# Kernel optimization log

Measured on AMD Instinct MI355X. Metric: run time of the kernel, lower is better.

Reference implementation:

```python
import jax, jax.numpy as jnp
import numpy as np

N_NODES = 100000


def _gcn_conv(x, edge_index, W, b, n_nodes):
    # PyG GCNConv with add_self_loops=True, default gcn_norm:
    #   out = D^{-1/2} (A + I) D^{-1/2} (x @ W) + b
    xw = x @ W  # [N, out_dim]
    src = jnp.concatenate([edge_index[0], jnp.arange(n_nodes)])
    dst = jnp.concatenate([edge_index[1], jnp.arange(n_nodes)])
    ones = jnp.ones(src.shape[0], dtype=x.dtype)
    deg = jax.ops.segment_sum(ones, dst, num_segments=n_nodes)  # includes self loops
    dinv = jnp.where(deg > 0, jax.lax.rsqrt(deg), 0.0)
    norm = dinv[src] * dinv[dst]  # [E + N]
    msgs = xw[src] * norm[:, None]  # gather + scale per edge
    out = jax.ops.segment_sum(msgs, dst, num_segments=n_nodes)
    return out + b


def setup_inputs() -> dict:
    key = jax.random.key(0)
    k1, k2, k3, k4 = jax.random.split(key, 4)
    N, E = N_NODES, 1600000
    in_dim, hid_dim, out_dim = 128, 128, 64
    x = jax.random.normal(k1, (N, in_dim), dtype=jnp.float32)
    edge_index = jax.random.randint(k2, (2, E), 0, N, dtype=jnp.int64)
    W1 = jax.random.normal(k3, (in_dim, hid_dim), dtype=jnp.float32) * (1.0 / np.sqrt(in_dim))
    b1 = jnp.zeros((hid_dim,), dtype=jnp.float32)
    W2 = jax.random.normal(k4, (hid_dim, out_dim), dtype=jnp.float32) * (1.0 / np.sqrt(hid_dim))
    b2 = jnp.zeros((out_dim,), dtype=jnp.float32)
    return {"x": x, "edge_index": edge_index, "W1": W1, "b1": b1, "W2": W2, "b2": b2}


def reference(x, edge_index, W1, b1, W2, b2):
    h = _gcn_conv(x, edge_index, W1, b1, N_NODES)
    out = _gcn_conv(h, edge_index, W2, b2, N_NODES)
    return out
```

## Files before the change

kernel.cpp:

```cpp
#include <hip/hip_runtime.h>

#define NNODES 100000
#define NBUCK ((NNODES + 127) >> 7)
#define CAPB 3072
#define BINCAP 16
#define GFILL 256

__device__ __forceinline__ float bf2f(unsigned short u) {
    unsigned int v = ((unsigned int)u) << 16;
    return __builtin_bit_cast(float, v);
}
__device__ __forceinline__ unsigned short f2bf(float f) {
    unsigned int u = __builtin_bit_cast(unsigned int, f);
    u += 0x7FFF + ((u >> 16) & 1);
    return (unsigned short)(u >> 16);
}


__global__ __launch_bounds__(512) void fill_wc(const int* __restrict__ ei, int E,
                                               int* __restrict__ gcur,
                                               int* __restrict__ seg) {
    __shared__ int lcnt[NBUCK];
    __shared__ int lbin[NBUCK * BINCAP];

    const int t = threadIdx.x;
    for (int i = t; i < NBUCK; i += 512) lcnt[i] = 0;
    __syncthreads();

    const int per = (E + GFILL - 1) / GFILL;
    const int e0 = blockIdx.x * per;
    const int e1 = min(e0 + per, E);

    for (int base = e0; base < e1; base += 512) {
        int e = base + t;
        if (e < e1) {
            int src = ei[e];
            int d = ei[E + e];
            int b = (unsigned)d >> 7;
            int p = (src << 7) | (d & 127);
            int pos = atomicAdd(&lcnt[b], 1);
            if (pos < BINCAP) {
                lbin[b * BINCAP + pos] = p;
            } else {
                int gp = atomicAdd(&gcur[b << 4], 1);
                if (gp < CAPB) seg[b * CAPB + gp] = p;
            }
        }
        __syncthreads();
        for (int bb = t; bb < NBUCK; bb += 512) {
            if (lcnt[bb] >= BINCAP) {
                int gp = atomicAdd(&gcur[bb << 4], BINCAP);
                if (gp + BINCAP <= CAPB) {
                    int* dp = seg + bb * CAPB + gp;
                    const int* sp = lbin + bb * BINCAP;
#pragma unroll
                    for (int j = 0; j < BINCAP; ++j) dp[j] = sp[j];
                }
                lcnt[bb] = 0;
            }
        }
        __syncthreads();
    }
    for (int bb = t; bb < NBUCK; bb += 512) {
        int c = min(lcnt[bb], BINCAP);
        if (c > 0) {
            int gp = atomicAdd(&gcur[bb << 4], c);
            int* dp = seg + bb * CAPB;
            const int* sp = lbin + bb * BINCAP;
            for (int j = 0; j < c && gp + j < CAPB; ++j) dp[gp + j] = sp[j];
        }
    }
}


__global__ __launch_bounds__(256) void stats_kernel(const int* __restrict__ gcur,
                                                    const int* __restrict__ seg,
                                                    float* __restrict__ dinv, int N) {
    __shared__ int cnt[128];
    const int t = threadIdx.x, b = blockIdx.x;
    if (t < 128) cnt[t] = 0;
    __syncthreads();
    int c = min(gcur[b << 4], CAPB);
    const int* sp = seg + b * CAPB;
    for (int i = t; i < c; i += 256) atomicAdd(&cnt[sp[i] & 127], 1);
    __syncthreads();
    int node = (b << 7) + t;
    if (t < 128 && node < N) dinv[node] = rsqrtf((float)cnt[t] + 1.0f);
}


__global__ __launch_bounds__(256) void w12_kernel(const float* __restrict__ W1,
                                                  const float* __restrict__ b1,
                                                  const float* __restrict__ W2,
                                                  float* __restrict__ W12,
                                                  float* __restrict__ bW2) {
    int j = threadIdx.x % 64;
    int r = threadIdx.x / 64;
    if (blockIdx.x < 32) {
        int i = blockIdx.x * 4 + r;
        float acc = 0.f;
        for (int k = 0; k < 128; ++k) acc += W1[i * 128 + k] * W2[k * 64 + j];
        W12[i * 64 + j] = acc;
    } else if (r == 0) {
        float acc = 0.f;
        for (int k = 0; k < 128; ++k) acc += b1[k] * W2[k * 64 + j];
        bW2[j] = acc;
    }
}


__global__ __launch_bounds__(256) void gemm_scale_bf(const float* __restrict__ X,
                                                     const float* __restrict__ W,
                                                     const float* __restrict__ dinv,
                                                     unsigned short* __restrict__ Ybf, int N) {
    constexpr int K = 128;
    constexpr int KP = K + 4;
    constexpr int OD = 64;
    constexpr int JG = OD / 4;
    constexpr int TR = 256 / JG;
    constexpr int ROWS = TR * 4;

    __shared__ float sW[K * OD];
    __shared__ float sX[ROWS * KP];

    const int tid = threadIdx.x;

    for (int i = tid; i < K * OD / 4; i += 256)
        ((float4*)sW)[i] = ((const float4*)W)[i];

    const int jg = tid % JG;
    const int tr = tid / JG;
    const int r0 = tr * 4;
    const int base = blockIdx.x * ROWS;

    const int k4 = (tid & 31) * 4;
    for (int rl = tid >> 5; rl < ROWS; rl += 8) {
        int row = base + rl;
        float4 v = make_float4(0.f, 0.f, 0.f, 0.f);
        if (row < N) v = *(const float4*)(X + (size_t)row * K + k4);
        *(float4*)(sX + rl * KP + k4) = v;
    }
    __syncthreads();

    float acc[4][4] = {{0.f}};
#pragma unroll 8
    for (int k = 0; k < K; ++k) {
        float4 w = *(const float4*)(sW + k * OD + jg * 4);
        float x0 = sX[(r0 + 0) * KP + k];
        float x1 = sX[(r0 + 1) * KP + k];
        float x2 = sX[(r0 + 2) * KP + k];
        float x3 = sX[(r0 + 3) * KP + k];
        acc[0][0] += x0 * w.x; acc[0][1] += x0 * w.y; acc[0][2] += x0 * w.z; acc[0][3] += x0 * w.w;
        acc[1][0] += x1 * w.x; acc[1][1] += x1 * w.y; acc[1][2] += x1 * w.z; acc[1][3] += x1 * w.w;
        acc[2][0] += x2 * w.x; acc[2][1] += x2 * w.y; acc[2][2] += x2 * w.z; acc[2][3] += x2 * w.w;
        acc[3][0] += x3 * w.x; acc[3][1] += x3 * w.y; acc[3][2] += x3 * w.z; acc[3][3] += x3 * w.w;
    }

#pragma unroll
    for (int i = 0; i < 4; ++i) {
        int row = base + r0 + i;
        if (row < N) {
            float sc = dinv[row];
            ushort4 o;
            o.x = f2bf(acc[i][0] * sc);
            o.y = f2bf(acc[i][1] * sc);
            o.z = f2bf(acc[i][2] * sc);
            o.w = f2bf(acc[i][3] * sc);
            *(ushort4*)(Ybf + (size_t)row * OD + jg * 4) = o;
        }
    }
}


template <bool FINAL>
__global__ __launch_bounds__(256) void agg_sort(const int* __restrict__ gcur,
                                                const int* __restrict__ seg,
                                                const unsigned short* __restrict__ Y,
                                                const float* __restrict__ dinv,
                                                const float* __restrict__ bW2,
                                                const float* __restrict__ b2,
                                                unsigned short* __restrict__ out_bf,
                                                float* __restrict__ out_f, int N) {
    __shared__ int el[CAPB];
    __shared__ int csr[CAPB];
    __shared__ int cnt[128], sh[128], rs[128], cur[128];

    const int t = threadIdx.x, b = blockIdx.x;
    const int total = min(gcur[b << 4], CAPB);

    if (t < 128) cnt[t] = 0;
    __syncthreads();
    {
        const int* sp = seg + b * CAPB;
        for (int i = t; i < total; i += 256) el[i] = sp[i];
    }
    __syncthreads();

    for (int i = t; i < total; i += 256) atomicAdd(&cnt[el[i] & 127], 1);
    __syncthreads();
    int v = (t < 128) ? cnt[t] : 0;
    if (t < 128) sh[t] = v;
    __syncthreads();
    for (int offp = 1; offp < 128; offp <<= 1) {
        int u = (t < 128 && t >= offp) ? sh[t - offp] : 0;
        __syncthreads();
        if (t < 128) sh[t] += u;
        __syncthreads();
    }
    if (t < 128) {
        int excl = sh[t] - v;
        rs[t] = excl;
        cur[t] = excl;
    }
    __syncthreads();
    for (int i = t; i < total; i += 256) {
        int p = el[i];
        int pos = atomicAdd(&cur[p & 127], 1);
        csr[pos] = (int)((unsigned)p >> 7);
    }
    __syncthreads();

    const int g = t >> 4, lane = t & 15, c4 = lane * 4;
    const int base = b << 7;

    for (int nl = g; nl < 128; nl += 16) {
        int node = base + nl;
        if (node >= N) continue;

        ushort4 sv = *(const ushort4*)(Y + (size_t)node * 64 + c4);
        float ax = bf2f(sv.x), ay = bf2f(sv.y), az = bf2f(sv.z), aw = bf2f(sv.w);
        float ds = 0.f;

        const int s0 = rs[nl];
        const int e0 = s0 + cnt[nl];
        int i = s0;
        for (; i + 4 <= e0; i += 4) {
            int a0 = csr[i + 0];
            int a1 = csr[i + 1];
            int a2 = csr[i + 2];
            int a3 = csr[i + 3];
            ushort4 v0 = *(const ushort4*)(Y + (size_t)a0 * 64 + c4);
            ushort4 v1 = *(const ushort4*)(Y + (size_t)a1 * 64 + c4);
            ushort4 v2 = *(const ushort4*)(Y + (size_t)a2 * 64 + c4);
            ushort4 v3 = *(const ushort4*)(Y + (size_t)a3 * 64 + c4);
            ax += bf2f(v0.x) + bf2f(v1.x) + bf2f(v2.x) + bf2f(v3.x);
            ay += bf2f(v0.y) + bf2f(v1.y) + bf2f(v2.y) + bf2f(v3.y);
            az += bf2f(v0.z) + bf2f(v1.z) + bf2f(v2.z) + bf2f(v3.z);
            aw += bf2f(v0.w) + bf2f(v1.w) + bf2f(v2.w) + bf2f(v3.w);
            if (FINAL && lane == 0)
                ds += dinv[a0] + dinv[a1] + dinv[a2] + dinv[a3];
        }
        for (; i < e0; ++i) {
            int a = csr[i];
            ushort4 vv = *(const ushort4*)(Y + (size_t)a * 64 + c4);
            ax += bf2f(vv.x); ay += bf2f(vv.y); az += bf2f(vv.z); aw += bf2f(vv.w);
            if (FINAL && lane == 0) ds += dinv[a];
        }

        float di = rsqrtf((float)cnt[nl] + 1.0f);
        if (FINAL) {
            float dsg = __shfl(ds, (g << 4), 64);
            float si = di * (di + dsg);
            float4 bb = *(const float4*)(bW2 + c4);
            float4 bv = *(const float4*)(b2 + c4);
            float4 o;
            o.x = di * ax + si * bb.x + bv.x;
            o.y = di * ay + si * bb.y + bv.y;
            o.z = di * az + si * bb.z + bv.z;
            o.w = di * aw + si * bb.w + bv.w;
            *(float4*)(out_f + (size_t)node * 64 + c4) = o;
        } else {
            float d2 = di * di;
            ushort4 o;
            o.x = f2bf(d2 * ax);
            o.y = f2bf(d2 * ay);
            o.z = f2bf(d2 * az);
            o.w = f2bf(d2 * aw);
            *(ushort4*)(out_bf + (size_t)node * 64 + c4) = o;
        }
    }
}


extern "C" void kernel_launch(void* const* d_in, const int* in_sizes, int n_in,
                              void* d_out, int out_size, void* d_ws, size_t ws_size,
                              hipStream_t stream) {
    const float* x  = (const float*)d_in[0];
    const int*   ei = (const int*)d_in[1];
    const float* W1 = (const float*)d_in[2];
    const float* b1 = (const float*)d_in[3];
    const float* W2 = (const float*)d_in[4];
    const float* b2 = (const float*)d_in[5];
    float* out = (float*)d_out;

    const int N = NNODES;
    const int E = in_sizes[1] / 2;

    float* ws   = (float*)d_ws;
    float* dinv = ws;
    float* W12  = dinv + N;
    float* bW2  = W12 + 8192;
    unsigned short* ybf = (unsigned short*)(bW2 + 64);
    unsigned short* zbf = ybf + (size_t)N * 64;
    int*  seg  = (int*)(zbf + (size_t)N * 64);
    int*  gcur = seg + (size_t)NBUCK * CAPB;

    hipMemsetAsync(gcur, 0, (size_t)NBUCK * 16 * sizeof(int), stream);

    fill_wc<<<GFILL, 512, 0, stream>>>(ei, E, gcur, seg);
    w12_kernel<<<33, 256, 0, stream>>>(W1, b1, W2, W12, bW2);
    stats_kernel<<<NBUCK, 256, 0, stream>>>(gcur, seg, dinv, N);

    gemm_scale_bf<<<(N + 63) / 64, 256, 0, stream>>>(x, W12, dinv, ybf, N);
    agg_sort<false><<<NBUCK, 256, 0, stream>>>(gcur, seg, ybf, dinv, nullptr, nullptr, zbf, nullptr, N);
    agg_sort<true><<<NBUCK, 256, 0, stream>>>(gcur, seg, zbf, dinv, bW2, b2, nullptr, out, N);
}
```

Measured before the change: 261.6 us.

## Sort buckets once into CSR, pipeline gathers, stream X directly in GEMM

```diff
diff --git a/kernel.cpp b/kernel.cpp
--- a/kernel.cpp
+++ b/kernel.cpp
@@ -73,19 +73,60 @@
 }
 
 
-__global__ __launch_bounds__(256) void stats_kernel(const int* __restrict__ gcur,
-                                                    const int* __restrict__ seg,
-                                                    float* __restrict__ dinv, int N) {
-    __shared__ int cnt[128];
+__global__ __launch_bounds__(512) void sortseg(const int* __restrict__ gcur,
+                                               int* __restrict__ seg,
+                                               float* __restrict__ dinv,
+                                               int* __restrict__ rsb,
+                                               int* __restrict__ cntb, int N) {
+    __shared__ int el[CAPB];
+    __shared__ int csr[CAPB];
+    __shared__ int cnt[128], sh[128], rs[128], cur[128];
+
     const int t = threadIdx.x, b = blockIdx.x;
+    const int total = min(gcur[b << 4], CAPB);
+
     if (t < 128) cnt[t] = 0;
     __syncthreads();
-    int c = min(gcur[b << 4], CAPB);
-    const int* sp = seg + b * CAPB;
-    for (int i = t; i < c; i += 256) atomicAdd(&cnt[sp[i] & 127], 1);
-    __syncthreads();
-    int node = (b << 7) + t;
-    if (t < 128 && node < N) dinv[node] = rsqrtf((float)cnt[t] + 1.0f);
+    {
+        const int* sp = seg + b * CAPB;
+        for (int i = t; i < total; i += 512) el[i] = sp[i];
+    }
+    __syncthreads();
+
+    for (int i = t; i < total; i += 512) atomicAdd(&cnt[el[i] & 127], 1);
+    __syncthreads();
+    int v = (t < 128) ? cnt[t] : 0;
+    if (t < 128) sh[t] = v;
+    __syncthreads();
+    for (int offp = 1; offp < 128; offp <<= 1) {
+        int u = (t < 128 && t >= offp) ? sh[t - offp] : 0;
+        __syncthreads();
+        if (t < 128) sh[t] += u;
+        __syncthreads();
+    }
+    if (t < 128) {
+        int excl = sh[t] - v;
+        rs[t] = excl;
+        cur[t] = excl;
+    }
+    __syncthreads();
+    for (int i = t; i < total; i += 512) {
+        int p = el[i];
+        int pos = atomicAdd(&cur[p & 127], 1);
+        csr[pos] = (int)((unsigned)p >> 7);
+    }
+    __syncthreads();
+
+    {
+        int* dp = seg + b * CAPB;
+        for (int i = t; i < total; i += 512) dp[i] = csr[i];
+    }
+    if (t < 128) {
+        rsb[b * 128 + t] = rs[t];
+        cntb[b * 128 + t] = cnt[t];
+        int node = (b << 7) + t;
+        if (node < N) dinv[node] = rsqrtf((float)cnt[t] + 1.0f);
+    }
 }
 
 
@@ -114,116 +155,90 @@
                                                      const float* __restrict__ dinv,
                                                      unsigned short* __restrict__ Ybf, int N) {
     constexpr int K = 128;
-    constexpr int KP = K + 4;
     constexpr int OD = 64;
-    constexpr int JG = OD / 4;
-    constexpr int TR = 256 / JG;
-    constexpr int ROWS = TR * 4;
 
     __shared__ float sW[K * OD];
-    __shared__ float sX[ROWS * KP];
 
     const int tid = threadIdx.x;
-
     for (int i = tid; i < K * OD / 4; i += 256)
         ((float4*)sW)[i] = ((const float4*)W)[i];
-
-    const int jg = tid % JG;
-    const int tr = tid / JG;
-    const int r0 = tr * 4;
-    const int base = blockIdx.x * ROWS;
-
-    const int k4 = (tid & 31) * 4;
-    for (int rl = tid >> 5; rl < ROWS; rl += 8) {
-        int row = base + rl;
-        float4 v = make_float4(0.f, 0.f, 0.f, 0.f);
-        if (row < N) v = *(const float4*)(X + (size_t)row * K + k4);
-        *(float4*)(sX + rl * KP + k4) = v;
-    }
-    __syncthreads();
+    __syncthreads();
+
+    const int jg = tid & 15;
+    const int tr = tid >> 4;
+    const int r0 = blockIdx.x * 64 + tr * 4;
+
+    const float* xr[4];
+#pragma unroll
+    for (int r = 0; r < 4; ++r) xr[r] = X + (size_t)min(r0 + r, N - 1) * K;
 
     float acc[4][4] = {{0.f}};
-#pragma unroll 8
-    for (int k = 0; k < K; ++k) {
-        float4 w = *(const float4*)(sW + k * OD + jg * 4);
-        float x0 = sX[(r0 + 0) * KP + k];
-        float x1 = sX[(r0 + 1) * KP + k];
-        float x2 = sX[(r0 + 2) * KP + k];
-        float x3 = sX[(r0 + 3) * KP + k];
-        acc[0][0] += x0 * w.x; acc[0][1] += x0 * w.y; acc[0][2] += x0 * w.z; acc[0][3] += x0 * w.w;
-        acc[1][0] += x1 * w.x; acc[1][1] += x1 * w.y; acc[1][2] += x1 * w.z; acc[1][3] += x1 * w.w;
-        acc[2][0] += x2 * w.x; acc[2][1] += x2 * w.y; acc[2][2] += x2 * w.z; acc[2][3] += x2 * w.w;
-        acc[3][0] += x3 * w.x; acc[3][1] += x3 * w.y; acc[3][2] += x3 * w.z; acc[3][3] += x3 * w.w;
-    }
-
-#pragma unroll
-    for (int i = 0; i < 4; ++i) {
-        int row = base + r0 + i;
+#pragma unroll 2
+    for (int k = 0; k < K; k += 4) {
+        float4 xv[4];
+#pragma unroll
+        for (int r = 0; r < 4; ++r) xv[r] = *(const float4*)(xr[r] + k);
+#pragma unroll
+        for (int kk = 0; kk < 4; ++kk) {
+            float4 w = *(const float4*)(sW + (k + kk) * OD + (jg << 2));
+#pragma unroll
+            for (int r = 0; r < 4; ++r) {
+                float xs = (&xv[r].x)[kk];
+                acc[r][0] += xs * w.x;
+                acc[r][1] += xs * w.y;
+                acc[r][2] += xs * w.z;
+                acc[r][3] += xs * w.w;
+            }
+        }
+    }
+
+#pragma unroll
+    for (int r = 0; r < 4; ++r) {
+        int row = r0 + r;
         if (row < N) {
             float sc = dinv[row];
             ushort4 o;
-            o.x = f2bf(acc[i][0] * sc);
-            o.y = f2bf(acc[i][1] * sc);
-            o.z = f2bf(acc[i][2] * sc);
-            o.w = f2bf(acc[i][3] * sc);
-            *(ushort4*)(Ybf + (size_t)row * OD + jg * 4) = o;
+            o.x = f2bf(acc[r][0] * sc);
+            o.y = f2bf(acc[r][1] * sc);
+            o.z = f2bf(acc[r][2] * sc);
+            o.w = f2bf(acc[r][3] * sc);
+            *(ushort4*)(Ybf + (size_t)row * OD + (jg << 2)) = o;
         }
     }
 }
 
 
 template <bool FINAL>
-__global__ __launch_bounds__(256) void agg_sort(const int* __restrict__ gcur,
-                                                const int* __restrict__ seg,
-                                                const unsigned short* __restrict__ Y,
-                                                const float* __restrict__ dinv,
-                                                const float* __restrict__ bW2,
-                                                const float* __restrict__ b2,
-                                                unsigned short* __restrict__ out_bf,
-                                                float* __restrict__ out_f, int N) {
-    __shared__ int el[CAPB];
-    __shared__ int csr[CAPB];
-    __shared__ int cnt[128], sh[128], rs[128], cur[128];
+__global__ __launch_bounds__(512) void agg_csr(const int* __restrict__ seg,
+                                               const int* __restrict__ rsb,
+                                               const int* __restrict__ cntb,
+                                               const unsigned short* __restrict__ Y,
+                                               const float* __restrict__ dinv,
+                                               const float* __restrict__ bW2,
+                                               const float* __restrict__ b2,
+                                               unsigned short* __restrict__ out_bf,
+                                               float* __restrict__ out_f, int N) {
+    __shared__ int csrS[CAPB];
+    __shared__ int rsS[128], cntS[128];
 
     const int t = threadIdx.x, b = blockIdx.x;
-    const int total = min(gcur[b << 4], CAPB);
-
-    if (t < 128) cnt[t] = 0;
-    __syncthreads();
+
+    if (t < 128) {
+        rsS[t] = rsb[b * 128 + t];
+        cntS[t] = cntb[b * 128 + t];
+    }
+    __syncthreads();
+    const int total = rsS[127] + cntS[127];
     {
         const int* sp = seg + b * CAPB;
-        for (int i = t; i < total; i += 256) el[i] = sp[i];
-    }
-    __syncthreads();
-
-    for (int i = t; i < total; i += 256) atomicAdd(&cnt[el[i] & 127], 1);
-    __syncthreads();
-    int v = (t < 128) ? cnt[t] : 0;
-    if (t < 128) sh[t] = v;
-    __syncthreads();
-    for (int offp = 1; offp < 128; offp <<= 1) {
-        int u = (t < 128 && t >= offp) ? sh[t - offp] : 0;
-        __syncthreads();
-        if (t < 128) sh[t] += u;
-        __syncthreads();
-    }
-    if (t < 128) {
-        int excl = sh[t] - v;
-        rs[t] = excl;
-        cur[t] = excl;
-    }
-    __syncthreads();
-    for (int i = t; i < total; i += 256) {
-        int p = el[i];
-        int pos = atomicAdd(&cur[p & 127], 1);
-        csr[pos] = (int)((unsigned)p >> 7);
+        for (int i = t; i < total; i += 512) csrS[i] = sp[i];
     }
     __syncthreads();
 
     const int g = t >> 4, lane = t & 15, c4 = lane * 4;
     const int base = b << 7;
 
-    for (int nl = g; nl < 128; nl += 16) {
+    for (int nl = g; nl < 128; nl += 32) {
         int node = base + nl;
         if (node >= N) continue;
 
@@ -231,36 +246,65 @@
         float ax = bf2f(sv.x), ay = bf2f(sv.y), az = bf2f(sv.z), aw = bf2f(sv.w);
         float ds = 0.f;
 
-        const int s0 = rs[nl];
-        const int e0 = s0 + cnt[nl];
+        const int s0 = rsS[nl];
+        const int ne = cntS[nl];
+        const int e0 = s0 + ne;
         int i = s0;
-        for (; i + 4 <= e0; i += 4) {
-            int a0 = csr[i + 0];
-            int a1 = csr[i + 1];
-            int a2 = csr[i + 2];
-            int a3 = csr[i + 3];
-            ushort4 v0 = *(const ushort4*)(Y + (size_t)a0 * 64 + c4);
-            ushort4 v1 = *(const ushort4*)(Y + (size_t)a1 * 64 + c4);
-            ushort4 v2 = *(const ushort4*)(Y + (size_t)a2 * 64 + c4);
-            ushort4 v3 = *(const ushort4*)(Y + (size_t)a3 * 64 + c4);
-            ax += bf2f(v0.x) + bf2f(v1.x) + bf2f(v2.x) + bf2f(v3.x);
-            ay += bf2f(v0.y) + bf2f(v1.y) + bf2f(v2.y) + bf2f(v3.y);
-            az += bf2f(v0.z) + bf2f(v1.z) + bf2f(v2.z) + bf2f(v3.z);
-            aw += bf2f(v0.w) + bf2f(v1.w) + bf2f(v2.w) + bf2f(v3.w);
-            if (FINAL && lane == 0)
-                ds += dinv[a0] + dinv[a1] + dinv[a2] + dinv[a3];
+        const int nch = ne >> 3;
+
+        if (nch > 0) {
+            ushort4 buf[8];
+            float dv = 0.f;
+#pragma unroll
+            for (int j = 0; j < 8; ++j)
+                buf[j] = *(const ushort4*)(Y + (size_t)csrS[s0 + j] * 64 + c4);
+            if (FINAL && lane < 8) dv = dinv[csrS[s0 + lane]];
+
+            for (int c = 1; c < nch; ++c) {
+                const int ib = s0 + (c << 3);
+                ushort4 nb[8];
+#pragma unroll
+                for (int j = 0; j < 8; ++j)
+                    nb[j] = *(const ushort4*)(Y + (size_t)csrS[ib + j] * 64 + c4);
+                float ndv = 0.f;
+                if (FINAL && lane < 8) ndv = dinv[csrS[ib + lane]];
+#pragma unroll
+                for (int j = 0; j < 8; ++j) {
+                    ax += bf2f(buf[j].x);
+                    ay += bf2f(buf[j].y);
+                    az += bf2f(buf[j].z);
+                    aw += bf2f(buf[j].w);
+                }
+                ds += dv;
+#pragma unroll
+                for (int j = 0; j < 8; ++j) buf[j] = nb[j];
+                dv = ndv;
+            }
+#pragma unroll
+            for (int j = 0; j < 8; ++j) {
+                ax += bf2f(buf[j].x);
+                ay += bf2f(buf[j].y);
+                az += bf2f(buf[j].z);
+                aw += bf2f(buf[j].w);
+            }
+            ds += dv;
+            i = s0 + (nch << 3);
         }
         for (; i < e0; ++i) {
-            int a = csr[i];
+            int a = csrS[i];
             ushort4 vv = *(const ushort4*)(Y + (size_t)a * 64 + c4);
             ax += bf2f(vv.x); ay += bf2f(vv.y); az += bf2f(vv.z); aw += bf2f(vv.w);
             if (FINAL && lane == 0) ds += dinv[a];
         }
 
-        float di = rsqrtf((float)cnt[nl] + 1.0f);
+        float di = rsqrtf((float)cntS[nl] + 1.0f);
         if (FINAL) {
-            float dsg = __shfl(ds, (g << 4), 64);
-            float si = di * (di + dsg);
+            float dt = ds;
+            dt += __shfl_xor(dt, 1, 64);
+            dt += __shfl_xor(dt, 2, 64);
+            dt += __shfl_xor(dt, 4, 64);
+            dt += __shfl_xor(dt, 8, 64);
+            float si = di * (di + dt);
             float4 bb = *(const float4*)(bW2 + c4);
             float4 bv = *(const float4*)(b2 + c4);
             float4 o;
@@ -304,14 +348,16 @@
     unsigned short* zbf = ybf + (size_t)N * 64;
     int*  seg  = (int*)(zbf + (size_t)N * 64);
     int*  gcur = seg + (size_t)NBUCK * CAPB;
+    int*  rsb  = gcur + (size_t)NBUCK * 16;
+    int*  cntb = rsb + (size_t)NBUCK * 128;
 
     hipMemsetAsync(gcur, 0, (size_t)NBUCK * 16 * sizeof(int), stream);
 
     fill_wc<<<GFILL, 512, 0, stream>>>(ei, E, gcur, seg);
     w12_kernel<<<33, 256, 0, stream>>>(W1, b1, W2, W12, bW2);
-    stats_kernel<<<NBUCK, 256, 0, stream>>>(gcur, seg, dinv, N);
+    sortseg<<<NBUCK, 512, 0, stream>>>(gcur, seg, dinv, rsb, cntb, N);
 
     gemm_scale_bf<<<(N + 63) / 64, 256, 0, stream>>>(x, W12, dinv, ybf, N);
-    agg_sort<false><<<NBUCK, 256, 0, stream>>>(gcur, seg, ybf, dinv, nullptr, nullptr, zbf, nullptr, N);
-    agg_sort<true><<<NBUCK, 256, 0, stream>>>(gcur, seg, zbf, dinv, bW2, b2, nullptr, out, N);
-}
+    agg_csr<false><<<NBUCK, 512, 0, stream>>>(seg, rsb, cntb, ybf, dinv, nullptr, nullptr, zbf, nullptr, N);
+    agg_csr<true><<<NBUCK, 512, 0, stream>>>(seg, rsb, cntb, zbf, dinv, bW2, b2, nullptr, out, N);
+}
```

After: 256.8 us. About the same (-1.8%).
